# Performance work log

Hardware: AMD Instinct MI355X
Metric: run time of the kernel (lower is better)

The kernel has to match this reference:

```python
import jax, jax.numpy as jnp
import numpy as np

# Layer configuration (from init_kwargs)
T = 32
TSEQ = jnp.linspace(1.0 / T, 1.0, T, dtype=jnp.float32)  # tseq grid
N_HOM_DIMS = 2      # dimensions = [0, 1]
KMAX = 4            # KK = [0,1,2,3] -> top-4 landscapes

B, N, P = 128, 256 * 256, 4096  # batch, grid cells, persistence pairs


def setup_inputs() -> dict:
    key = jax.random.key(0)
    k1, k2, k3, k4 = jax.random.split(key, 4)
    fun_value = jax.random.uniform(k1, (B, N), dtype=jnp.float32)
    birth_idx = jax.random.randint(k2, (B, P), 0, N, dtype=jnp.int32)
    death_idx = jax.random.randint(k3, (B, P), 0, N, dtype=jnp.int32)
    pair_dim = jax.random.randint(k4, (B, P), 0, N_HOM_DIMS, dtype=jnp.int32)
    return {"fun_value": fun_value, "birth_idx": birth_idx,
            "death_idx": death_idx, "pair_dim": pair_dim}


def reference(fun_value, birth_idx, death_idx, pair_dim):
    # Gather birth/death filtration values of each persistence pair
    # (this is fun_value[locationBirth] / fun_value[locationDeath]).
    b = jnp.take_along_axis(fun_value, birth_idx, axis=-1)   # [B, P]
    d = jnp.take_along_axis(fun_value, death_idx, axis=-1)   # [B, P]
    # Tent functions: fab[b, t, p] = max(min(tseq[t] - birth_p, death_p - tseq[t]), 0)
    fab = jnp.maximum(
        jnp.minimum(TSEQ[None, :, None] - b[:, None, :],
                    d[:, None, :] - TSEQ[None, :, None]),
        0.0)                                                  # [B, T, P]
    # Restrict pairs to each homology dimension; out-of-dim pairs become the
    # zero padding the original code uses in its fab buffer.
    dims = jnp.arange(N_HOM_DIMS, dtype=pair_dim.dtype)
    in_dim = pair_dim[:, None, None, :] == dims[None, :, None, None]  # [B, D, 1, P]
    fab_d = jnp.where(in_dim, fab[:, None, :, :], 0.0)        # [B, D, T, P]
    # Landscape = top-KMAX values over pairs (== -sort(-fab)[..., KK]).
    land, _ = jax.lax.top_k(fab_d, KMAX)                      # [B, D, T, KMAX]
    return land
```

## Files before the change

kernel.cpp:

```cpp
#include <hip/hip_runtime.h>

#define B_ 128
#define N_ 65536
#define P_ 4096
#define T_ 32
#define D_ 2
#define K_ 4
#define S_ 16
#define PPB 256
#define CHUNK (N_ / S_)

#define INS(v0, v1, v2, v3, val)                                  \
    {                                                             \
        float _x = fminf(v0, val); v0 = fmaxf(v0, val);           \
        float _y = fminf(v1, _x);  v1 = fmaxf(v1, _x);            \
        float _z = fminf(v2, _y);  v2 = fmaxf(v2, _y);            \
        v3 = fmaxf(v3, _z);                                       \
    }

__global__ __launch_bounds__(256, 8) void fused_scan(
        const float* __restrict__ fun,
        const int* __restrict__ bidx,
        const int* __restrict__ didx,
        const int* __restrict__ pdim,
        float* __restrict__ partial) {
    __shared__ __align__(16) float2 bdS[PPB + 8];
    __shared__ int cnt0S[4];
    __shared__ int cnt1S[4];
    __shared__ __align__(16) float4 mrg[4][64];

    int bid   = blockIdx.x;
    int xcd   = bid & 7;
    int seq   = bid >> 3;
    int batch = xcd * 16 + (seq & 15);
    int slice = seq >> 4;

    int tid  = threadIdx.x;
    int lane = tid & 63;
    int wave = tid >> 6;

    const float* f = fun + (size_t)batch * N_;
    int p = batch * P_ + slice * PPB + tid;

    const float4* pf = (const float4*)(f + slice * CHUNK);
    float4 w0 = pf[tid];
    float4 w1 = pf[tid + 256];
    float4 w2 = pf[tid + 512];
    float4 w3 = pf[tid + 768];
    int bi = bidx[p];
    int di = didx[p];
    int pd = pdim[p];

    float ka = (w0.x + w0.y + w0.z + w0.w) + (w1.x + w1.y + w1.z + w1.w)
             + (w2.x + w2.y + w2.z + w2.w) + (w3.x + w3.y + w3.z + w3.w);
    asm volatile("" :: "v"(ka));
    __syncthreads();
    __builtin_amdgcn_sched_barrier(0);

    float b = f[bi], d = f[di];

    bool k0 = (d > b) && (pd == 0);
    bool k1 = (d > b) && (pd == 1);
    unsigned long long bal0 = __ballot(k0);
    unsigned long long bal1 = __ballot(k1);
    if (lane == 0) {
        cnt0S[wave] = __popcll(bal0);
        cnt1S[wave] = __popcll(bal1);
    }
    __syncthreads();

    int pre0 = 0, pre1 = 0, tot0 = 0, tot1 = 0;
    #pragma unroll
    for (int c = 0; c < 4; ++c) {
        int c0 = cnt0S[c], c1 = cnt1S[c];
        if (c < wave) { pre0 += c0; pre1 += c1; }
        tot0 += c0; tot1 += c1;
    }
    int A  = (tot0 + 3) & ~3;
    int L1 = (tot1 + 3) & ~3;

    unsigned long long lm = (1ull << lane) - 1ull;
    if (k0) bdS[pre0 + __popcll(bal0 & lm)]     = make_float2(b, d);
    if (k1) bdS[A + pre1 + __popcll(bal1 & lm)] = make_float2(b, d);
    if (tid < A - tot0)                  bdS[tot0 + tid]           = make_float2(4.f, -4.f);
    if (tid >= 4 && tid - 4 < L1 - tot1) bdS[A + tot1 + (tid - 4)] = make_float2(4.f, -4.f);
    __syncthreads();

    int half = lane >> 5;
    int t    = lane & 31;
    float tf = (float)(t + 1) * 0.03125f;

    float a0 = 0.f, a1 = 0.f, a2 = 0.f, a3 = 0.f;
    float c0 = 0.f, c1 = 0.f, c2 = 0.f, c3 = 0.f;

    const float2* bd0 = bdS + 2 * half;
    #pragma unroll 2
    for (int j = wave * 4; j < A; j += 16) {
        float4 q = *(const float4*)(bd0 + j);
        float v0 = fminf(tf - q.x, q.y - tf);
        float v1 = fminf(tf - q.z, q.w - tf);
        INS(a0, a1, a2, a3, v0);
        INS(a0, a1, a2, a3, v1);
    }
    #pragma unroll 2
    for (int j = wave * 4; j < L1; j += 16) {
        float4 q = *(const float4*)(bd0 + A + j);
        float v0 = fminf(tf - q.x, q.y - tf);
        float v1 = fminf(tf - q.z, q.w - tf);
        INS(c0, c1, c2, c3, v0);
        INS(c0, c1, c2, c3, v1);
    }

    float u0 = (half == 0) ? a0 : c0, x0 = (half == 0) ? c0 : a0;
    float u1 = (half == 0) ? a1 : c1, x1 = (half == 0) ? c1 : a1;
    float u2 = (half == 0) ? a2 : c2, x2 = (half == 0) ? c2 : a2;
    float u3 = (half == 0) ? a3 : c3, x3 = (half == 0) ? c3 : a3;
    float q;
    q = __shfl_xor(x0, 32); INS(u0, u1, u2, u3, q);
    q = __shfl_xor(x1, 32); INS(u0, u1, u2, u3, q);
    q = __shfl_xor(x2, 32); INS(u0, u1, u2, u3, q);
    q = __shfl_xor(x3, 32); INS(u0, u1, u2, u3, q);

    mrg[wave][lane] = make_float4(u0, u1, u2, u3);
    __syncthreads();

    if (wave == 0) {
        float v0 = 0.f, v1 = 0.f, v2 = 0.f, v3 = 0.f;
        #pragma unroll
        for (int w = 0; w < 4; ++w) {
            float4 m = mrg[w][lane];
            INS(v0, v1, v2, v3, m.x);
            INS(v0, v1, v2, v3, m.y);
            INS(v0, v1, v2, v3, m.z);
            INS(v0, v1, v2, v3, m.w);
        }
        ((float4*)partial)[((size_t)batch * S_ + slice) * 64 + lane] =
            make_float4(v0, v1, v2, v3);
    }
}

__global__ __launch_bounds__(256) void final_merge(
        const float* __restrict__ partial,
        float* __restrict__ out) {
    int tid   = blockIdx.x * 256 + threadIdx.x;
    int batch = tid >> 6;
    int combo = tid & 63;
    const float4* src = (const float4*)partial + (size_t)batch * S_ * 64 + combo;
    float v0 = 0.f, v1 = 0.f, v2 = 0.f, v3 = 0.f;
    #pragma unroll
    for (int s = 0; s < S_; ++s) {
        float4 p = src[(size_t)s * 64];
        INS(v0, v1, v2, v3, p.x);
        INS(v0, v1, v2, v3, p.y);
        INS(v0, v1, v2, v3, p.z);
        INS(v0, v1, v2, v3, p.w);
    }
    ((float4*)out)[tid] = make_float4(v0, v1, v2, v3);
}

extern "C" void kernel_launch(void* const* d_in, const int* in_sizes, int n_in,
                              void* d_out, int out_size, void* d_ws, size_t ws_size,
                              hipStream_t stream) {
    const float* fun  = (const float*)d_in[0];
    const int*   bidx = (const int*)d_in[1];
    const int*   didx = (const int*)d_in[2];
    const int*   pdim = (const int*)d_in[3];
    float* out = (float*)d_out;

    float* partial = (float*)d_ws;

    fused_scan<<<B_ * S_, 256, 0, stream>>>(fun, bidx, didx, pdim, partial);
    final_merge<<<(B_ * 64) / 256, 256, 0, stream>>>(partial, out);
}
```

Measured before the change: 89.10 us.

## Fuse final merge into scan kernel via last-block atomic counter; drop chunk prefetch

Result: slower. 159.7 us (+79.3%).

```diff
diff --git a/kernel.cpp b/kernel.cpp
--- a/kernel.cpp
+++ b/kernel.cpp
@@ -8,7 +8,6 @@
 #define K_ 4
 #define S_ 16
 #define PPB 256
-#define CHUNK (N_ / S_)
 
 #define INS(v0, v1, v2, v3, val)                                  \
     {                                                             \
@@ -23,11 +22,14 @@
         const int* __restrict__ bidx,
         const int* __restrict__ didx,
         const int* __restrict__ pdim,
-        float* __restrict__ partial) {
+        float* __restrict__ partial,
+        int* __restrict__ done,
+        float* __restrict__ out) {
     __shared__ __align__(16) float2 bdS[PPB + 8];
     __shared__ int cnt0S[4];
     __shared__ int cnt1S[4];
     __shared__ __align__(16) float4 mrg[4][64];
+    __shared__ int lastS;
 
     int bid   = blockIdx.x;
     int xcd   = bid & 7;
@@ -42,21 +44,9 @@
     const float* f = fun + (size_t)batch * N_;
     int p = batch * P_ + slice * PPB + tid;
 
-    const float4* pf = (const float4*)(f + slice * CHUNK);
-    float4 w0 = pf[tid];
-    float4 w1 = pf[tid + 256];
-    float4 w2 = pf[tid + 512];
-    float4 w3 = pf[tid + 768];
     int bi = bidx[p];
     int di = didx[p];
     int pd = pdim[p];
-
-    float ka = (w0.x + w0.y + w0.z + w0.w) + (w1.x + w1.y + w1.z + w1.w)
-             + (w2.x + w2.y + w2.z + w2.w) + (w3.x + w3.y + w3.z + w3.w);
-    asm volatile("" :: "v"(ka));
-    __syncthreads();
-    __builtin_amdgcn_sched_barrier(0);
-
     float b = f[bi], d = f[di];
 
     bool k0 = (d > b) && (pd == 0);
@@ -136,26 +126,30 @@
         }
         ((float4*)partial)[((size_t)batch * S_ + slice) * 64 + lane] =
             make_float4(v0, v1, v2, v3);
+        __threadfence();
     }
-}
+    __syncthreads();
 
-__global__ __launch_bounds__(256) void final_merge(
-        const float* __restrict__ partial,
-        float* __restrict__ out) {
-    int tid   = blockIdx.x * 256 + threadIdx.x;
-    int batch = tid >> 6;
-    int combo = tid & 63;
-    const float4* src = (const float4*)partial + (size_t)batch * S_ * 64 + combo;
-    float v0 = 0.f, v1 = 0.f, v2 = 0.f, v3 = 0.f;
-    #pragma unroll
-    for (int s = 0; s < S_; ++s) {
-        float4 p = src[(size_t)s * 64];
-        INS(v0, v1, v2, v3, p.x);
-        INS(v0, v1, v2, v3, p.y);
-        INS(v0, v1, v2, v3, p.z);
-        INS(v0, v1, v2, v3, p.w);
+    if (tid == 0) {
+        int old = __hip_atomic_fetch_add(&done[batch], 1,
+                                         __ATOMIC_ACQ_REL,
+                                         __HIP_MEMORY_SCOPE_AGENT);
+        lastS = (old == S_ - 1);
     }
-    ((float4*)out)[tid] = make_float4(v0, v1, v2, v3);
+    __syncthreads();
+    if (lastS && tid < 64) {
+        const float4* src = (const float4*)partial + (size_t)batch * S_ * 64 + tid;
+        float v0 = 0.f, v1 = 0.f, v2 = 0.f, v3 = 0.f;
+        #pragma unroll
+        for (int s = 0; s < S_; ++s) {
+            float4 m = src[(size_t)s * 64];
+            INS(v0, v1, v2, v3, m.x);
+            INS(v0, v1, v2, v3, m.y);
+            INS(v0, v1, v2, v3, m.z);
+            INS(v0, v1, v2, v3, m.w);
+        }
+        ((float4*)out)[(size_t)batch * 64 + tid] = make_float4(v0, v1, v2, v3);
+    }
 }
 
 extern "C" void kernel_launch(void* const* d_in, const int* in_sizes, int n_in,
@@ -168,7 +162,9 @@
     float* out = (float*)d_out;
 
     float* partial = (float*)d_ws;
+    int*   done    = (int*)((char*)d_ws + (size_t)B_ * S_ * 64 * sizeof(float4));
 
-    fused_scan<<<B_ * S_, 256, 0, stream>>>(fun, bidx, didx, pdim, partial);
-    final_merge<<<(B_ * 64) / 256, 256, 0, stream>>>(partial, out);
+    hipMemsetAsync(done, 0, B_ * sizeof(int), stream);
+    fused_scan<<<B_ * S_, 256, 0, stream>>>(fun, bidx, didx, pdim,
+                                            partial, done, out);
 }
```
